# Kernel optimization log

Measured on AMD Instinct MI355X. Metric: run time of the kernel, lower is better.

Reference implementation:

```python
import jax, jax.numpy as jnp
import numpy as np

N_HEAD = 16


def setup_inputs() -> dict:
    key = jax.random.key(0)
    k1, k2, k3 = jax.random.split(key, 3)
    B, T, N = 4, 2048, 1024
    x = jax.random.normal(k1, (B, T, N), dtype=jnp.float32)
    W_attn = jax.random.normal(k2, (N, 3 * N), dtype=jnp.float32) * (1.0 / np.sqrt(N))
    b_attn = jnp.zeros((3 * N,), dtype=jnp.float32)
    W_proj = jax.random.normal(k3, (N, N), dtype=jnp.float32) * (1.0 / np.sqrt(N))
    b_proj = jnp.zeros((N,), dtype=jnp.float32)
    return {"x": x, "W_attn": W_attn, "b_attn": b_attn, "W_proj": W_proj, "b_proj": b_proj}


def reference(x, W_attn, b_attn, W_proj, b_proj):
    B, T, N = x.shape
    H = N_HEAD
    Dh = N // H
    qkv = x @ W_attn + b_attn                      # [B, T, 3N]
    q, k, v = jnp.split(qkv, 3, axis=2)
    # [B, H, T, Dh]
    q = q.reshape(B, T, H, Dh).transpose(0, 2, 1, 3)
    k = k.reshape(B, T, H, Dh).transpose(0, 2, 1, 3)
    v = v.reshape(B, T, H, Dh).transpose(0, 2, 1, 3)
    att = jnp.einsum('bhqd,bhkd->bhqk', q, k) / (Dh ** 0.5)
    mask = jnp.tril(jnp.ones((T, T), dtype=bool))
    att = jnp.where(mask[None, None], att, jnp.finfo(x.dtype).min)
    att = jax.nn.softmax(att, axis=-1)
    y = jnp.einsum('bhqk,bhkd->bhqd', att, v)      # [B, H, T, Dh]
    y = y.transpose(0, 2, 1, 3).reshape(B, T, N)
    return y @ W_proj + b_proj
```

## Files before the change

kernel.cpp:

```cpp
#include <hip/hip_runtime.h>
#include <hip/hip_bf16.h>


typedef __attribute__((ext_vector_type(8))) short short8;
typedef __attribute__((ext_vector_type(4))) float f32x4;
typedef __attribute__((ext_vector_type(16))) float f32x16;

#define MFMA16(a, b, c) __builtin_amdgcn_mfma_f32_16x16x32_bf16((a), (b), (c), 0, 0, 0)
#define MFMA32(a, b, c) __builtin_amdgcn_mfma_f32_32x32x16_bf16((a), (b), (c), 0, 0, 0)

#if defined(__has_builtin)
#if __has_builtin(__builtin_amdgcn_exp2f)
#define EXP2(x) __builtin_amdgcn_exp2f(x)
#endif
#endif
#ifndef EXP2
#define EXP2(x) exp2f(x)
#endif

__device__ __forceinline__ void gload_lds16(const void* g, void* l) {
  __builtin_amdgcn_global_load_lds(
      (const __attribute__((address_space(1))) unsigned int*)g,
      (__attribute__((address_space(3))) unsigned int*)l, 16, 0, 0);
}

__device__ __forceinline__ unsigned pack_bf16x2(float lo, float hi) {
  unsigned ulo = __float_as_uint(lo) + 0x8000u;
  unsigned uhi = __float_as_uint(hi) + 0x8000u;
  return __builtin_amdgcn_perm(uhi, ulo, 0x07060302u);
}

__device__ __forceinline__ unsigned short bf16u(float f) {
  return (unsigned short)((__float_as_uint(f) + 0x8000u) >> 16);
}

__global__ void prep_kernel(const float* __restrict__ x, unsigned* __restrict__ Xb,
                            const float* __restrict__ Wa, __hip_bfloat16* __restrict__ WaT,
                            const float* __restrict__ Wp, __hip_bfloat16* __restrict__ WpT) {
  __shared__ float tile[32][33];
  const int tid = threadIdx.x;
  int blk = blockIdx.x;
  if (blk >= 4096) {
    int i = (blk - 4096) * 256 + tid;
    float4 v = ((const float4*)x)[i];
    uint2 o;
    o.x = pack_bf16x2(v.x, v.y);
    o.y = pack_bf16x2(v.z, v.w);
    ((uint2*)Xb)[i] = o;
    return;
  }
  const float* src;
  __hip_bfloat16* dst;
  int R, C, bx, by;
  if (blk < 3072) {
    src = Wa; dst = WaT; R = 1024; C = 3072; bx = blk % 96; by = blk / 96;
  } else {
    blk -= 3072;
    src = Wp; dst = WpT; R = 1024; C = 1024; bx = blk & 31; by = blk >> 5;
  }
  const int tx = tid & 31, ty = tid >> 5;
  const int c0 = bx * 32, r0 = by * 32;
#pragma unroll
  for (int i = 0; i < 32; i += 8)
    tile[ty + i][tx] = src[(long)(r0 + ty + i) * C + c0 + tx];
  __syncthreads();
#pragma unroll
  for (int i = 0; i < 32; i += 8)
    dst[(long)(c0 + ty + i) * R + r0 + tx] = __float2bfloat16(tile[tx][ty + i]);
}

template <int EPI>
__global__ __launch_bounds__(256, 2) void gemm_bt(
    const __hip_bfloat16* __restrict__ A, const __hip_bfloat16* __restrict__ Bt,
    const float* __restrict__ bias, void* o0, void* o1, void* o2, int N, int K) {
  __shared__ alignas(16) char smem[34816];
  short8 (*As)[8] = (short8(*)[8])smem;
  short8 (*Bs)[8] = (short8(*)[8])(smem + 16384);
  unsigned short (*C16)[136] = (unsigned short(*)[136])smem;
  float (*C32)[132] = (float(*)[132])smem;

  const int tid = threadIdx.x;
  const int lane = tid & 63, w = tid >> 6;
  const int l15 = lane & 15, quad = lane >> 4;
  const int wm = (w >> 1) * 64, wn = (w & 1) * 64;
  const int rowBase = blockIdx.y * 128;
  const int colBase = blockIdx.x * 128;
  const int sr8 = lane >> 3;
  const int scc = (lane & 7) ^ sr8;

  f32x4 acc[4][4];
#pragma unroll
  for (int mi = 0; mi < 4; ++mi)
#pragma unroll
    for (int ni = 0; ni < 4; ++ni)
      acc[mi][ni] = {0.f, 0.f, 0.f, 0.f};

  for (int k0 = 0; k0 < K; k0 += 64) {
    __syncthreads();
#pragma unroll
    for (int p = 0; p < 4; ++p) {
      const int rb = p * 32 + w * 8;
      const int row = rb + sr8;
      gload_lds16(A + (rowBase + row) * K + k0 + scc * 8, &As[rb][0]);
      gload_lds16(Bt + (colBase + row) * K + k0 + scc * 8, &Bs[rb][0]);
    }
    __syncthreads();
#pragma unroll
    for (int kc = 0; kc < 2; ++kc) {
      short8 af[4], bf[4];
#pragma unroll
      for (int mi = 0; mi < 4; ++mi) {
        int row = wm + mi * 16 + l15;
        af[mi] = As[row][(kc * 4 + quad) ^ (row & 7)];
      }
#pragma unroll
      for (int ni = 0; ni < 4; ++ni) {
        int row = wn + ni * 16 + l15;
        bf[ni] = Bs[row][(kc * 4 + quad) ^ (row & 7)];
      }
#pragma unroll
      for (int mi = 0; mi < 4; ++mi)
#pragma unroll
        for (int ni = 0; ni < 4; ++ni)
          acc[mi][ni] = MFMA16(af[mi], bf[ni], acc[mi][ni]);
    }
  }

  float bcol[4];
#pragma unroll
  for (int ni = 0; ni < 4; ++ni) bcol[ni] = bias[colBase + wn + ni * 16 + l15];

  if (EPI == 0) {
    const int which = colBase >> 10;
    const int b = rowBase >> 11;
    const int tt0 = rowBase & 2047;
    const int n1base = colBase & 1023;
    const float osc = (which == 0) ? 0.180336880111f : 1.0f;
    __syncthreads();
    if (which != 2) {
#pragma unroll
      for (int mi = 0; mi < 4; ++mi)
#pragma unroll
        for (int ni = 0; ni < 4; ++ni)
#pragma unroll
          for (int r = 0; r < 4; ++r)
            C16[wm + mi * 16 + quad * 4 + r][wn + ni * 16 + l15] =
                bf16u((acc[mi][ni][r] + bcol[ni]) * osc);
    } else {
#pragma unroll
      for (int mi = 0; mi < 4; ++mi)
#pragma unroll
        for (int ni = 0; ni < 4; ++ni)
#pragma unroll
          for (int r = 0; r < 4; ++r)
            C16[wn + ni * 16 + l15][wm + mi * 16 + quad * 4 + r] =
                bf16u(acc[mi][ni][r] + bcol[ni]);
    }
    __syncthreads();
    unsigned short* o = (unsigned short*)(which == 0 ? o0 : which == 1 ? o1 : o2);
    if (which != 2) {
#pragma unroll
      for (int j = 0; j < 8; ++j) {
        int flat = j * 256 + tid;
        int trow = flat >> 4, ch = flat & 15;
        int h = (n1base + ((ch & 8) << 3)) >> 6;
        long addr = ((long)((b * 16 + h) * 2048 + tt0 + trow)) * 64 + (ch & 7) * 8;
        *(short8*)&o[addr] = *(const short8*)&C16[trow][ch * 8];
      }
    } else {
#pragma unroll
      for (int j = 0; j < 8; ++j) {
        int flat = j * 256 + tid;
        int dcol = flat >> 4, ch = flat & 15;
        int h = (n1base + (dcol & 64)) >> 6;
        long addr = ((long)((b * 16 + h) * 64 + (dcol & 63))) * 2048 + tt0 + ch * 8;
        *(short8*)&o[addr] = *(const short8*)&C16[dcol][ch * 8];
      }
    }
  } else {
    float* out = (float*)o0;
    for (int p = 0; p < 2; ++p) {
      __syncthreads();
      if ((w >> 1) == p) {
#pragma unroll
        for (int mi = 0; mi < 4; ++mi)
#pragma unroll
          for (int ni = 0; ni < 4; ++ni)
#pragma unroll
            for (int r = 0; r < 4; ++r)
              C32[mi * 16 + quad * 4 + r][wn + ni * 16 + l15] =
                  acc[mi][ni][r] + bcol[ni];
      }
      __syncthreads();
#pragma unroll
      for (int j = 0; j < 8; ++j) {
        int flat = j * 256 + tid;
        int row = flat >> 5, ch = flat & 31;
        float4 v4 = *(const float4*)&C32[row][ch * 4];
        *(float4*)&out[(long)(rowBase + p * 64 + row) * N + colBase + ch * 4] = v4;
      }
    }
  }
}

__global__ __launch_bounds__(256, 3) void attn_kernel(
    const __hip_bfloat16* __restrict__ Q, const __hip_bfloat16* __restrict__ K,
    const __hip_bfloat16* __restrict__ Vt, __hip_bfloat16* __restrict__ Y, int T) {
  __shared__ short8 Ks[3][64][8];
  __shared__ short8 Vs[3][64][8];
  const int tid = threadIdx.x;
  const int w = tid >> 6, lane = tid & 63;
  const int c31 = lane & 31, half = lane >> 5;
  const int rsw = c31 & 7;
  const int idx = blockIdx.x;
  const int bh = idx & 63;
  const int b = bh >> 4, h = bh & 15;
  const int qsel = idx >> 6;
  const int qq = qsel >> 2, qp = qsel & 3;
  const int jt = (qq == 0) ? 15 - qp : (qq == 1) ? 8 + qp : (qq == 2) ? 4 + qp : 3 - qp;

  const int qrow0 = jt * 128 + w * 32;
  const __hip_bfloat16* Qp = Q + (long)bh * T * 64;
  const __hip_bfloat16* Kp = K + (long)bh * T * 64;
  const __hip_bfloat16* Vp = Vt + (long)bh * 64 * T;

  const int sr8 = lane >> 3;
  const int scc = (lane & 7) ^ sr8;

  short8 qf[4];
#pragma unroll
  for (int s = 0; s < 4; ++s)
    qf[s] = *(const short8*)(Qp + (qrow0 + c31) * 64 + s * 16 + half * 8);

  f32x16 czero;
#pragma unroll
  for (int i = 0; i < 16; ++i) czero[i] = 0.f;
  f32x16 oacc[2];
#pragma unroll
  for (int g = 0; g < 2; ++g) oacc[g] = czero;
  float lsum = 0.f;
  const int myq = qrow0 + c31;
  const int nkt = 2 * jt + 2;
  const int my_nkt = 2 * jt + 1 + (w >> 1);
  const int my_diag = my_nkt - 1;

#define STAGE_ATTN(buf, kbase)                                                 \
  do {                                                                         \
    const int rb_ = w * 16;                                                    \
    gload_lds16(Kp + ((kbase) + rb_ + sr8) * 64 + scc * 8, &Ks[buf][rb_][0]);  \
    gload_lds16(Kp + ((kbase) + rb_ + 8 + sr8) * 64 + scc * 8,                 \
                &Ks[buf][rb_ + 8][0]);                                         \
    gload_lds16(Vp + (long)(rb_ + sr8) * T + (kbase) + scc * 8,                \
                &Vs[buf][rb_][0]);                                             \
    gload_lds16(Vp + (long)(rb_ + 8 + sr8) * T + (kbase) + scc * 8,            \
                &Vs[buf][rb_ + 8][0]);                                         \
  } while (0)

  STAGE_ATTN(0, 0);
  STAGE_ATTN(1, 64);
  int bcur = 0;

  for (int kt = 0; kt < nkt; ++kt) {
    if (kt < nkt - 1)
      asm volatile("s_waitcnt vmcnt(4)" ::: "memory");
    else
      asm volatile("s_waitcnt vmcnt(0)" ::: "memory");
    __builtin_amdgcn_s_barrier();
    __builtin_amdgcn_sched_barrier(0);

    if (kt + 2 < nkt) {
      const int bs = (bcur >= 1) ? bcur - 1 : 2;
      STAGE_ATTN(bs, (kt + 2) * 64);
    }

    if (kt < my_nkt) {
      const int kb = kt * 64;
      short8 pb[4];
#pragma unroll
      for (int g = 0; g < 2; ++g) {
        f32x16 z = MFMA32(Ks[bcur][g * 32 + c31][half ^ rsw], qf[0], czero);
#pragma unroll
        for (int s = 1; s < 4; ++s) {
          short8 af = Ks[bcur][g * 32 + c31][(s * 2 + half) ^ rsw];
          z = MFMA32(af, qf[s], z);
        }
        if (kt == my_diag) {
#pragma unroll
          for (int r = 0; r < 16; ++r) {
            int key = kb + g * 32 + (r & 3) + 8 * (r >> 2) + 4 * half;
            if (key > myq) z[r] = -INFINITY;
          }
        }
        unsigned pk[8];
#pragma unroll
        for (int i = 0; i < 8; ++i) {
          float p0 = EXP2(z[2 * i]);
          float p1 = EXP2(z[2 * i + 1]);
          lsum += p0 + p1;
          pk[i] = pack_bf16x2(p0, p1);
        }
#pragma unroll
        for (int s = 0; s < 2; ++s) {
          auto r0 = __builtin_amdgcn_permlane32_swap(pk[4 * s + 0], pk[4 * s + 2],
                                                     false, false);
          auto r1 = __builtin_amdgcn_permlane32_swap(pk[4 * s + 1], pk[4 * s + 3],
                                                     false, false);
          union { unsigned u[4]; short8 s8; } cv;
          cv.u[0] = r0[0]; cv.u[1] = r1[0]; cv.u[2] = r0[1]; cv.u[3] = r1[1];
          pb[g * 2 + s] = cv.s8;
        }
      }
#pragma unroll
      for (int dg = 0; dg < 2; ++dg)
#pragma unroll
        for (int S = 0; S < 4; ++S) {
          short8 vf = Vs[bcur][dg * 32 + c31][(S * 2 + half) ^ rsw];
          oacc[dg] = MFMA32(vf, pb[S], oacc[dg]);
        }
    }
    bcur = (bcur == 2) ? 0 : bcur + 1;
  }

  lsum += __shfl_xor(lsum, 32);

  const float inv = 1.0f / lsum;
  unsigned short* Yu = (unsigned short*)Y;
  const long rowoff = ((long)(b * 2048 + qrow0 + c31)) * 1024 + h * 64;
#pragma unroll
  for (int dg = 0; dg < 2; ++dg)
#pragma unroll
    for (int rg = 0; rg < 4; ++rg) {
      uint2 o;
      o.x = pack_bf16x2(oacc[dg][rg * 4 + 0] * inv, oacc[dg][rg * 4 + 1] * inv);
      o.y = pack_bf16x2(oacc[dg][rg * 4 + 2] * inv, oacc[dg][rg * 4 + 3] * inv);
      *(uint2*)&Yu[rowoff + dg * 32 + half * 4 + rg * 8] = o;
    }
}

extern "C" void kernel_launch(void* const* d_in, const int* in_sizes, int n_in,
                              void* d_out, int out_size, void* d_ws, size_t ws_size,
                              hipStream_t stream) {
  const float* x  = (const float*)d_in[0];
  const float* Wa = (const float*)d_in[1];
  const float* ba = (const float*)d_in[2];
  const float* Wp = (const float*)d_in[3];
  const float* bp = (const float*)d_in[4];
  float* out = (float*)d_out;

  char* ws = (char*)d_ws;
  __hip_bfloat16* Xb  = (__hip_bfloat16*)(ws);
  __hip_bfloat16* WaT = (__hip_bfloat16*)(ws + 16777216);
  __hip_bfloat16* WpT = (__hip_bfloat16*)(ws + 23068672);
  __hip_bfloat16* Qb  = (__hip_bfloat16*)(ws + 25165824);
  __hip_bfloat16* Kb  = (__hip_bfloat16*)(ws + 41943040);
  __hip_bfloat16* Vtb = (__hip_bfloat16*)(ws + 58720256);
  __hip_bfloat16* Yb  = (__hip_bfloat16*)(ws + 75497472);
  if (ws_size < 92274688) return;

  prep_kernel<<<12288, 256, 0, stream>>>(x, (unsigned*)Xb, Wa, WaT, Wp, WpT);
  gemm_bt<0><<<dim3(24, 64), 256, 0, stream>>>(Xb, WaT, ba, Qb, Kb, Vtb, 3072, 1024);
  attn_kernel<<<dim3(1024), dim3(256), 0, stream>>>(Qb, Kb, Vtb, Yb, 2048);
  gemm_bt<1><<<dim3(8, 64), 256, 0, stream>>>(Yb, WpT, bp, out, nullptr, nullptr, 1024, 1024);
}
```

Before: 222.7 us.

## Double per-wave query tile in attention to reuse K/V fragments across two query groups

Each wave now processes 64 query rows as two 32-row groups, sharing every K and V LDS fragment between two MFMAs. Block query tile grows to 256 rows and the grid halves, with a new tile ordering to balance causal work. This cuts LDS reads and barrier overhead per unit of compute but raises register pressure, lowers occupancy (launch bounds 2), and reduces block count, which may worsen tail imbalance.

```diff
diff --git a/kernel.cpp b/kernel.cpp
--- a/kernel.cpp
+++ b/kernel.cpp
@@ -203,7 +203,7 @@
   }
 }
 
-__global__ __launch_bounds__(256, 3) void attn_kernel(
+__global__ __launch_bounds__(256, 2) void attn_kernel(
     const __hip_bfloat16* __restrict__ Q, const __hip_bfloat16* __restrict__ K,
     const __hip_bfloat16* __restrict__ Vt, __hip_bfloat16* __restrict__ Y, int T) {
   __shared__ short8 Ks[3][64][8];
@@ -216,10 +216,9 @@
   const int bh = idx & 63;
   const int b = bh >> 4, h = bh & 15;
   const int qsel = idx >> 6;
-  const int qq = qsel >> 2, qp = qsel & 3;
-  const int jt = (qq == 0) ? 15 - qp : (qq == 1) ? 8 + qp : (qq == 2) ? 4 + qp : 3 - qp;
-
-  const int qrow0 = jt * 128 + w * 32;
+  const int jt = (qsel < 4) ? 7 - 2 * qsel : 2 * (qsel - 4);
+
+  const int qrow0 = jt * 256 + w * 64;
   const __hip_bfloat16* Qp = Q + (long)bh * T * 64;
   const __hip_bfloat16* Kp = K + (long)bh * T * 64;
   const __hip_bfloat16* Vp = Vt + (long)bh * 64 * T;
@@ -227,21 +226,25 @@
   const int sr8 = lane >> 3;
   const int scc = (lane & 7) ^ sr8;
 
-  short8 qf[4];
+  short8 qf[4][2];
 #pragma unroll
   for (int s = 0; s < 4; ++s)
-    qf[s] = *(const short8*)(Qp + (qrow0 + c31) * 64 + s * 16 + half * 8);
+#pragma unroll
+    for (int qg = 0; qg < 2; ++qg)
+      qf[s][qg] = *(const short8*)(Qp + (qrow0 + qg * 32 + c31) * 64 + s * 16 + half * 8);
 
   f32x16 czero;
 #pragma unroll
   for (int i = 0; i < 16; ++i) czero[i] = 0.f;
-  f32x16 oacc[2];
-#pragma unroll
-  for (int g = 0; g < 2; ++g) oacc[g] = czero;
-  float lsum = 0.f;
+  f32x16 oacc[2][2];
+#pragma unroll
+  for (int dg = 0; dg < 2; ++dg)
+#pragma unroll
+    for (int qg = 0; qg < 2; ++qg) oacc[dg][qg] = czero;
+  float lsum[2] = {0.f, 0.f};
   const int myq = qrow0 + c31;
-  const int nkt = 2 * jt + 2;
-  const int my_nkt = 2 * jt + 1 + (w >> 1);
+  const int nkt = 4 * jt + 4;
+  const int my_nkt = 4 * jt + w + 1;
   const int my_diag = my_nkt - 1;
 
 #define STAGE_ATTN(buf, kbase)                                                 \
@@ -275,39 +278,47 @@
 
     if (kt < my_nkt) {
       const int kb = kt * 64;
-      short8 pb[4];
-#pragma unroll
-      for (int g = 0; g < 2; ++g) {
-        f32x16 z = MFMA32(Ks[bcur][g * 32 + c31][half ^ rsw], qf[0], czero);
+      short8 pb[2][4];
+#pragma unroll
+      for (int kg = 0; kg < 2; ++kg) {
+        short8 af0 = Ks[bcur][kg * 32 + c31][half ^ rsw];
+        f32x16 z0 = MFMA32(af0, qf[0][0], czero);
+        f32x16 z1 = MFMA32(af0, qf[0][1], czero);
 #pragma unroll
         for (int s = 1; s < 4; ++s) {
-          short8 af = Ks[bcur][g * 32 + c31][(s * 2 + half) ^ rsw];
-          z = MFMA32(af, qf[s], z);
+          short8 af = Ks[bcur][kg * 32 + c31][(s * 2 + half) ^ rsw];
+          z0 = MFMA32(af, qf[s][0], z0);
+          z1 = MFMA32(af, qf[s][1], z1);
         }
         if (kt == my_diag) {
 #pragma unroll
           for (int r = 0; r < 16; ++r) {
-            int key = kb + g * 32 + (r & 3) + 8 * (r >> 2) + 4 * half;
-            if (key > myq) z[r] = -INFINITY;
+            int key = kb + kg * 32 + (r & 3) + 8 * (r >> 2) + 4 * half;
+            if (key > myq) z0[r] = -INFINITY;
+            if (key > myq + 32) z1[r] = -INFINITY;
           }
         }
-        unsigned pk[8];
-#pragma unroll
-        for (int i = 0; i < 8; ++i) {
-          float p0 = EXP2(z[2 * i]);
-          float p1 = EXP2(z[2 * i + 1]);
-          lsum += p0 + p1;
-          pk[i] = pack_bf16x2(p0, p1);
-        }
-#pragma unroll
-        for (int s = 0; s < 2; ++s) {
-          auto r0 = __builtin_amdgcn_permlane32_swap(pk[4 * s + 0], pk[4 * s + 2],
-                                                     false, false);
-          auto r1 = __builtin_amdgcn_permlane32_swap(pk[4 * s + 1], pk[4 * s + 3],
-                                                     false, false);
-          union { unsigned u[4]; short8 s8; } cv;
-          cv.u[0] = r0[0]; cv.u[1] = r1[0]; cv.u[2] = r0[1]; cv.u[3] = r1[1];
-          pb[g * 2 + s] = cv.s8;
+#pragma unroll
+        for (int qg = 0; qg < 2; ++qg) {
+          const f32x16& z = qg ? z1 : z0;
+          unsigned pk[8];
+#pragma unroll
+          for (int i = 0; i < 8; ++i) {
+            float p0 = EXP2(z[2 * i]);
+            float p1 = EXP2(z[2 * i + 1]);
+            lsum[qg] += p0 + p1;
+            pk[i] = pack_bf16x2(p0, p1);
+          }
+#pragma unroll
+          for (int s2 = 0; s2 < 2; ++s2) {
+            auto r0 = __builtin_amdgcn_permlane32_swap(pk[4 * s2 + 0], pk[4 * s2 + 2],
+                                                       false, false);
+            auto r1 = __builtin_amdgcn_permlane32_swap(pk[4 * s2 + 1], pk[4 * s2 + 3],
+                                                       false, false);
+            union { unsigned u[4]; short8 s8; } cv;
+            cv.u[0] = r0[0]; cv.u[1] = r1[0]; cv.u[2] = r0[1]; cv.u[3] = r1[1];
+            pb[qg][kg * 2 + s2] = cv.s8;
+          }
         }
       }
 #pragma unroll
@@ -315,26 +326,31 @@
 #pragma unroll
         for (int S = 0; S < 4; ++S) {
           short8 vf = Vs[bcur][dg * 32 + c31][(S * 2 + half) ^ rsw];
-          oacc[dg] = MFMA32(vf, pb[S], oacc[dg]);
+          oacc[dg][0] = MFMA32(vf, pb[0][S], oacc[dg][0]);
+          oacc[dg][1] = MFMA32(vf, pb[1][S], oacc[dg][1]);
         }
     }
     bcur = (bcur == 2) ? 0 : bcur + 1;
   }
 
-  lsum += __shfl_xor(lsum, 32);
-
-  const float inv = 1.0f / lsum;
+  lsum[0] += __shfl_xor(lsum[0], 32);
+  lsum[1] += __shfl_xor(lsum[1], 32);
+
   unsigned short* Yu = (unsigned short*)Y;
-  const long rowoff = ((long)(b * 2048 + qrow0 + c31)) * 1024 + h * 64;
-#pragma unroll
-  for (int dg = 0; dg < 2; ++dg)
-#pragma unroll
-    for (int rg = 0; rg < 4; ++rg) {
-      uint2 o;
-      o.x = pack_bf16x2(oacc[dg][rg * 4 + 0] * inv, oacc[dg][rg * 4 + 1] * inv);
-      o.y = pack_bf16x2(oacc[dg][rg * 4 + 2] * inv, oacc[dg][rg * 4 + 3] * inv);
-      *(uint2*)&Yu[rowoff + dg * 32 + half * 4 + rg * 8] = o;
-    }
+#pragma unroll
+  for (int qg = 0; qg < 2; ++qg) {
+    const float inv = 1.0f / lsum[qg];
+    const long rowoff = ((long)(b * 2048 + qrow0 + qg * 32 + c31)) * 1024 + h * 64;
+#pragma unroll
+    for (int dg = 0; dg < 2; ++dg)
+#pragma unroll
+      for (int rg = 0; rg < 4; ++rg) {
+        uint2 o;
+        o.x = pack_bf16x2(oacc[dg][qg][rg * 4 + 0] * inv, oacc[dg][qg][rg * 4 + 1] * inv);
+        o.y = pack_bf16x2(oacc[dg][qg][rg * 4 + 2] * inv, oacc[dg][qg][rg * 4 + 3] * inv);
+        *(uint2*)&Yu[rowoff + dg * 32 + half * 4 + rg * 8] = o;
+      }
+  }
 }
 
 extern "C" void kernel_launch(void* const* d_in, const int* in_sizes, int n_in,
@@ -359,6 +375,6 @@
 
   prep_kernel<<<12288, 256, 0, stream>>>(x, (unsigned*)Xb, Wa, WaT, Wp, WpT);
   gemm_bt<0><<<dim3(24, 64), 256, 0, stream>>>(Xb, WaT, ba, Qb, Kb, Vtb, 3072, 1024);
-  attn_kernel<<<dim3(1024), dim3(256), 0, stream>>>(Qb, Kb, Vtb, Yb, 2048);
+  attn_kernel<<<dim3(512), dim3(256), 0, stream>>>(Qb, Kb, Vtb, Yb, 2048);
   gemm_bt<1><<<dim3(8, 64), 256, 0, stream>>>(Yb, WpT, bp, out, nullptr, nullptr, 1024, 1024);
 }
```

Result: slower. 237.9 us (+6.8%).
